# Optimization experiments

Measured on AMD Instinct MI355X. Metric: run time of the kernel, lower is better.

## Reference

```python
import jax, jax.numpy as jnp
import numpy as np
import math

B, NIN, DIM, QK, GS, L, BINS = 512, 128, 512, 128, 32, 2, 100
HID = int(DIM * 2.0)
G = NIN // GS
ROT = 32  # rotary dim = min(32, query_key_dim)
EPS = 1e-5


def setup_inputs() -> dict:
    key = jax.random.key(0)
    ks = jax.random.split(key, 8)
    r = jax.random.normal
    return {
        "tokens": jax.random.randint(ks[0], (B, NIN), 0, BINS),
        "emb": r(ks[1], (NIN, BINS, DIM), jnp.float32) * 0.02,
        "pos_emb": r(ks[2], (NIN, DIM), jnp.float32) * 0.01,
        "norm_g": jnp.ones((L,), jnp.float32),
        "Wh": r(ks[3], (L, DIM, 2 * HID), jnp.float32) / math.sqrt(DIM),
        "bh": jnp.zeros((L, 2 * HID), jnp.float32),
        "Wqk": r(ks[4], (L, DIM, QK), jnp.float32) / math.sqrt(DIM),
        "bqk": jnp.zeros((L, QK), jnp.float32),
        "gamma": r(ks[5], (L, 4, QK), jnp.float32) * 0.02,
        "beta": jnp.zeros((L, 4, QK), jnp.float32),
        "rp": r(ks[6], (L, 32), jnp.float32) * 0.02,
        "Wout": r(ks[7], (L, HID, DIM), jnp.float32) / math.sqrt(HID),
        "bout": jnp.zeros((L, DIM), jnp.float32),
        "ln_g": jnp.ones((DIM,), jnp.float32),
        "ln_b": jnp.zeros((DIM,), jnp.float32),
    }


def _t5_buckets(n, num_buckets=32, max_distance=128):
    # causal T5 relative position buckets, computed statically
    pos = np.arange(n)
    rel = pos[None, :] - pos[:, None]
    neg = np.maximum(-rel, 0)
    max_exact = num_buckets // 2
    vl = max_exact + (np.log(np.maximum(neg, 1) / max_exact) / np.log(max_distance / max_exact) * (num_buckets - max_exact)).astype(np.int64)
    vl = np.minimum(vl, num_buckets - 1)
    return jnp.asarray(np.where(neg < max_exact, neg, vl))


def _rotary_cos_sin(n):
    inv = 1.0 / (10000.0 ** (np.arange(0, ROT, 2) / ROT))
    f = np.einsum('i,j->ij', np.arange(n), inv)  # [n, ROT/2]
    f = np.repeat(f, 2, axis=-1)                 # interleaved-pair freqs [n, ROT]
    return jnp.asarray(np.cos(f), jnp.float32), jnp.asarray(np.sin(f), jnp.float32)


def _apply_rotary(x, cos, sin):
    xr, xp = x[..., :ROT], x[..., ROT:]
    x2 = xr.reshape(*xr.shape[:-1], ROT // 2, 2)
    rh = jnp.stack((-x2[..., 1], x2[..., 0]), axis=-1).reshape(xr.shape)
    return jnp.concatenate([xr * cos + rh * sin, xp], axis=-1)


def reference(tokens, emb, pos_emb, norm_g, Wh, bh, Wqk, bqk, gamma, beta, rp, Wout, bout, ln_g, ln_b):
    # per-column embedding lookup + positional embedding
    x = emb[jnp.arange(NIN)[None, :], tokens] + pos_emb  # [B, NIN, DIM]
    buckets = _t5_buckets(GS)
    cos, sin = _rotary_cos_sin(NIN)
    t5_scale = QK ** 0.5
    causal_mask = jnp.triu(jnp.ones((GS, GS), bool), 1)

    def grp(t):
        return t.reshape(B, G, GS, t.shape[-1])

    def layer(h, p):
        ng, Wh_l, bh_l, Wqk_l, bqk_l, gm, bt, rp_l, Wo_l, bo_l = p
        # ScaleNorm
        nrm = jnp.linalg.norm(h, axis=-1, keepdims=True) * DIM ** -0.5
        nx = h / jnp.maximum(nrm, EPS) * ng
        # shift_tokens: shift first half of features by one position
        xs, xp = nx[..., :DIM // 2], nx[..., DIM // 2:]
        xs = jnp.pad(xs, ((0, 0), (1, 0), (0, 0)))[:, :-1]
        nx = jnp.concatenate([xs, xp], axis=-1)
        hid = jax.nn.silu(nx @ Wh_l + bh_l)
        v, gate = hid[..., :HID], hid[..., HID:]
        qk = jax.nn.silu(nx @ Wqk_l + bqk_l)
        qs = qk[..., None, :] * gm + bt  # [B, NIN, 4, QK]
        quad_q = _apply_rotary(qs[..., 0, :], cos, sin)
        lin_q = _apply_rotary(qs[..., 1, :], cos, sin)
        quad_k = _apply_rotary(qs[..., 2, :], cos, sin)
        lin_k = _apply_rotary(qs[..., 3, :], cos, sin)
        qq, lq, kk, lk, vg = map(grp, (quad_q, lin_q, quad_k, lin_k, v))
        # grouped quadratic attention with ReLU^2 attn fn and T5 rel-pos bias
        sim = jnp.einsum('bgid,bgjd->bgij', qq, kk) / GS + rp_l[buckets] * t5_scale
        attn = jnp.square(jax.nn.relu(sim))
        attn = jnp.where(causal_mask, 0.0, attn)
        quad_out = jnp.einsum('bgij,bgje->bgie', attn, vg)
        # causal linear attention across groups (shifted cumsum of kv stats)
        lin_kv = jnp.einsum('bgnd,bgne->bgde', lk, vg) / GS
        lin_kv = jnp.cumsum(lin_kv, axis=1)
        lin_kv = jnp.pad(lin_kv, ((0, 0), (1, 0), (0, 0), (0, 0)))[:, :-1]
        lin_out = jnp.einsum('bgde,bgnd->bgne', lin_kv, lq)
        out = gate * (quad_out + lin_out).reshape(B, NIN, HID)
        return out @ Wo_l + bo_l + h, None

    x, _ = jax.lax.scan(layer, x, (norm_g, Wh, bh, Wqk, bqk, gamma, beta, rp, Wout, bout))
    mu = x.mean(-1, keepdims=True)
    var = x.var(-1, keepdims=True)
    return (x - mu) / jnp.sqrt(var + EPS) * ln_g + ln_b
```

## Files before the change

### kernel.cpp

```cpp
#include <hip/hip_runtime.h>
#include <hip/hip_bf16.h>
#include <math.h>
#include <stdint.h>

#define BB   512
#define NIN  128
#define DIMD 512
#define QKD  128
#define GSZ  32
#define GRP  4
#define HID  1024
#define HID2 2048
#define NFUSE 2176
#define ROT  32
#define NLAYER 2
#define EPSF 1e-5f
#define BINS 100

typedef __bf16 bf16x8 __attribute__((ext_vector_type(8)));
typedef float  f32x4  __attribute__((ext_vector_type(4)));
typedef float  f32x16 __attribute__((ext_vector_type(16)));

__device__ __forceinline__ unsigned short f2bf(float f) {
    union { float f; uint32_t u; } v; v.f = f;
    return (unsigned short)((v.u + 0x7FFFu + ((v.u >> 16) & 1u)) >> 16);
}
__device__ __forceinline__ float bf2f(unsigned short h) {
    union { uint32_t u; float f; } v; v.u = ((uint32_t)h) << 16;
    return v.f;
}

__global__ void k_embed(const int* __restrict__ tokens, const float* __restrict__ emb,
                        const float* __restrict__ pos, float* __restrict__ h) {
    int bn = blockIdx.x;
    int n  = bn % NIN;
    int tok = tokens[bn];
    const float4* e4 = (const float4*)(emb + ((size_t)n * BINS + tok) * DIMD);
    const float4* p4 = (const float4*)(pos + (size_t)n * DIMD);
    float4* h4 = (float4*)(h + (size_t)bn * DIMD);
    int t = threadIdx.x;
    float4 a = e4[t], b = p4[t];
    h4[t] = make_float4(a.x + b.x, a.y + b.y, a.z + b.z, a.w + b.w);
}

__global__ void k_nxf(const float* __restrict__ h, unsigned short* __restrict__ nx,
                      const float* __restrict__ ngp) {
    int bn = blockIdx.x; int n = bn % NIN;
    int t = threadIdx.x;
    float4 v = ((const float4*)(h + (size_t)bn * DIMD))[t];
    float sq = v.x * v.x + v.y * v.y + v.z * v.z + v.w * v.w;
    __shared__ float red[2];
    #pragma unroll
    for (int o = 32; o; o >>= 1) sq += __shfl_down(sq, o);
    int lane = t & 63, w = t >> 6;
    if (lane == 0) red[w] = sq;
    __syncthreads();
    float s = red[0] + red[1];
    float nrm = sqrtf(s) * (1.0f / sqrtf((float)DIMD));
    float sc = ngp[0] / fmaxf(nrm, EPSF);
    ushort4 o = make_ushort4(f2bf(v.x * sc), f2bf(v.y * sc), f2bf(v.z * sc), f2bf(v.w * sc));
    if (t < 64) {
        if (n == 0)
            ((ushort4*)(nx + (size_t)bn * DIMD))[t] = make_ushort4(0, 0, 0, 0);
        if (n != NIN - 1)
            ((ushort4*)(nx + (size_t)(bn + 1) * DIMD))[t] = o;
    } else {
        ((ushort4*)(nx + (size_t)bn * DIMD))[t] = o;
    }
}

__global__ void k_wcast(const float* __restrict__ W, unsigned short* __restrict__ Wt,
                        int K, int N) {
    int idx = blockIdx.x * 256 + threadIdx.x;
    int total = N * (K / 8);
    if (idx >= total) return;
    int kb = idx / N, n = idx % N;
    #pragma unroll
    for (int j = 0; j < 8; ++j)
        Wt[(size_t)n * K + kb * 8 + j] = f2bf(W[(size_t)(kb * 8 + j) * N + n]);
}

#define GLOAD_LDS(gp, lp) __builtin_amdgcn_global_load_lds( \
    (const __attribute__((address_space(1))) uint32_t*)(gp), \
    (__attribute__((address_space(3))) uint32_t*)(lp), 16, 0, 0)

__global__ __launch_bounds__(256) void k_gemm_f(
        const unsigned short* __restrict__ A,
        const unsigned short* __restrict__ Bt,
        const float* __restrict__ bias0,
        const float* __restrict__ bias1,
        float* __restrict__ Cf,
        unsigned short* __restrict__ vTp,
        unsigned short* __restrict__ gatep,
        int M, int N, int K) {
    __shared__ unsigned short As[3][128 * 32];
    __shared__ unsigned short Bs[3][128 * 32];
    const int tid = threadIdx.x;

    int flat = blockIdx.y * gridDim.x + blockIdx.x;
    int nwg  = gridDim.x * gridDim.y;
    int q = nwg >> 3, r = nwg & 7;
    int xcd = flat & 7, idx = flat >> 3;
    int swz = (xcd < r ? xcd * (q + 1) : r * (q + 1) + (xcd - r) * q) + idx;
    const int bxi = swz % gridDim.x, byi = swz / gridDim.x;
    const int bm = byi * 128, bn = bxi * 128;

    const int lane = tid & 63, wave = tid >> 6;
    const int wm = (wave >> 1) * 64, wn = (wave & 1) * 64;
    const int l15 = lane & 15, l4 = lane >> 4;

    f32x4 acc[4][4];
    #pragma unroll
    for (int i = 0; i < 4; ++i)
        #pragma unroll
        for (int j = 0; j < 4; ++j) acc[i][j] = (f32x4){0.f, 0.f, 0.f, 0.f};

    const int rowA = tid >> 2;
    const int colB = (tid & 3) * 16;
    const char* gA = (const char*)(A  + (size_t)(bm + rowA) * K) + colB;
    const char* gB = (const char*)(Bt + (size_t)(bn + rowA) * K) + colB;
    const size_t stride64 = (size_t)64 * K * 2;

    #define STAGEF(bi, k0) do { \
        const char* sA_ = gA + (size_t)(k0) * 2; \
        const char* sB_ = gB + (size_t)(k0) * 2; \
        GLOAD_LDS(sA_,            &As[bi][tid * 8]); \
        GLOAD_LDS(sA_ + stride64, &As[bi][tid * 8 + 2048]); \
        GLOAD_LDS(sB_,            &Bs[bi][tid * 8]); \
        GLOAD_LDS(sB_ + stride64, &Bs[bi][tid * 8 + 2048]); \
    } while (0)

    const int NIT = K / 32;
    STAGEF(0, 0);
    STAGEF(1, 32);

    int cur = 0;
    for (int t = 0; t < NIT; ++t) {
        asm volatile("s_waitcnt lgkmcnt(0)" ::: "memory");
        if (t + 1 < NIT) asm volatile("s_waitcnt vmcnt(4)" ::: "memory");
        else             asm volatile("s_waitcnt vmcnt(0)" ::: "memory");
        __builtin_amdgcn_s_barrier();

        if (t + 2 < NIT) {
            int tgt = cur + 2; if (tgt >= 3) tgt -= 3;
            STAGEF(tgt, (t + 2) * 32);
        }

        bf16x8 af[4], bfr[4];
        #pragma unroll
        for (int f = 0; f < 4; ++f) {
            af[f]  = *(const bf16x8*)&As[cur][(wm + f * 16 + l15) * 32 + l4 * 8];
            bfr[f] = *(const bf16x8*)&Bs[cur][(wn + f * 16 + l15) * 32 + l4 * 8];
        }
        __builtin_amdgcn_s_setprio(1);
        #pragma unroll
        for (int i = 0; i < 4; ++i)
            #pragma unroll
            for (int j = 0; j < 4; ++j)
                acc[i][j] = __builtin_amdgcn_mfma_f32_16x16x32_bf16(af[i], bfr[j], acc[i][j], 0, 0, 0);
        __builtin_amdgcn_s_setprio(0);

        cur = (cur == 2) ? 0 : cur + 1;
    }
    #undef STAGEF

    #pragma unroll
    for (int i = 0; i < 4; ++i) {
        const int n0 = wm + i * 16 + l4 * 4;
        #pragma unroll
        for (int j = 0; j < 4; ++j) {
            const int col = bn + wn + j * 16 + l15;
            float bsv = (col < 2 * HID) ? bias0[col] : bias1[col - 2 * HID];
            float vv[4];
            #pragma unroll
            for (int rr = 0; rr < 4; ++rr) {
                float v = acc[i][j][rr] + bsv;
                vv[rr] = v / (1.0f + __expf(-v));
            }
            if (col < HID) {
                ushort4 o = make_ushort4(f2bf(vv[0]), f2bf(vv[1]), f2bf(vv[2]), f2bf(vv[3]));
                *(ushort4*)&vTp[((size_t)byi * HID + col) * NIN + n0] = o;
            } else if (col < 2 * HID) {
                #pragma unroll
                for (int rr = 0; rr < 4; ++rr)
                    gatep[(size_t)(bm + n0 + rr) * HID + (col - HID)] = f2bf(vv[rr]);
            } else {
                #pragma unroll
                for (int rr = 0; rr < 4; ++rr)
                    Cf[(size_t)(bm + n0 + rr) * QKD + (col - 2 * HID)] = vv[rr];
            }
        }
    }
}

__global__ __launch_bounds__(256, 2) void k_gemm_o(
        const unsigned short* __restrict__ A,
        const unsigned short* __restrict__ Bt,
        const float* __restrict__ bias0,
        const float* __restrict__ resid,
        float* __restrict__ Cf,
        int M, int N, int K) {
    __shared__ unsigned short As[2][256 * 32];
    __shared__ unsigned short Bs[2][128 * 32];
    const int tid = threadIdx.x;

    int flat = blockIdx.y * gridDim.x + blockIdx.x;
    int nwg  = gridDim.x * gridDim.y;
    int q = nwg >> 3, r = nwg & 7;
    int xcd = flat & 7, idx = flat >> 3;
    int swz = (xcd < r ? xcd * (q + 1) : r * (q + 1) + (xcd - r) * q) + idx;
    const int bxi = swz % gridDim.x, byi = swz / gridDim.x;
    const int bm = byi * 256, bn = bxi * 128;

    const int lane = tid & 63, wave = tid >> 6;
    const int l15 = lane & 15, l4 = lane >> 4;

    f32x4 acc[4][8];
    #pragma unroll
    for (int i = 0; i < 4; ++i)
        #pragma unroll
        for (int j = 0; j < 8; ++j) acc[i][j] = (f32x4){0.f, 0.f, 0.f, 0.f};

    const int rowA = tid >> 2;
    const int colO = (tid & 3) * 16;
    const int colS = colO ^ ((rowA & 3) << 4);
    const char* gA = (const char*)(A  + (size_t)(bm + rowA) * K) + colS;
    const char* gB = (const char*)(Bt + (size_t)(bn + rowA) * K) + colS;
    const size_t stride64 = (size_t)64 * K * 2;

    #define STAGEO(bi, k0) do { \
        const char* sA_ = gA + (size_t)(k0) * 2; \
        const char* sB_ = gB + (size_t)(k0) * 2; \
        GLOAD_LDS(sA_,                 &As[bi][tid * 8]); \
        GLOAD_LDS(sA_ +     stride64,  &As[bi][tid * 8 + 2048]); \
        GLOAD_LDS(sA_ + 2 * stride64,  &As[bi][tid * 8 + 4096]); \
        GLOAD_LDS(sA_ + 3 * stride64,  &As[bi][tid * 8 + 6144]); \
        GLOAD_LDS(sB_,                 &Bs[bi][tid * 8]); \
        GLOAD_LDS(sB_ +     stride64,  &Bs[bi][tid * 8 + 2048]); \
    } while (0)

    const int NIT = K / 32;
    STAGEO(0, 0);
    STAGEO(1, 32);

    for (int t = 0; t < NIT; ++t) {
        const int cur = t & 1;
        if (t + 1 < NIT) asm volatile("s_waitcnt vmcnt(6)" ::: "memory");
        else             asm volatile("s_waitcnt vmcnt(0)" ::: "memory");
        __builtin_amdgcn_s_barrier();
        __builtin_amdgcn_sched_barrier(0);

        bf16x8 af[4], bfr[8];
        #pragma unroll
        for (int f = 0; f < 4; ++f) {
            int rA = wave * 64 + f * 16 + l15;
            af[f] = *(const bf16x8*)&As[cur][rA * 32 + ((l4 ^ (rA & 3)) << 3)];
        }
        #pragma unroll
        for (int c = 0; c < 8; ++c) {
            int rB = c * 16 + l15;
            bfr[c] = *(const bf16x8*)&Bs[cur][rB * 32 + ((l4 ^ (rB & 3)) << 3)];
        }
        asm volatile("s_waitcnt lgkmcnt(0)" ::: "memory");
        __builtin_amdgcn_sched_barrier(0);
        __builtin_amdgcn_s_barrier();
        __builtin_amdgcn_sched_barrier(0);
        if (t + 2 < NIT) STAGEO(cur, (t + 2) * 32);

        __builtin_amdgcn_s_setprio(1);
        #pragma unroll
        for (int f = 0; f < 4; ++f)
            #pragma unroll
            for (int c = 0; c < 8; ++c)
                acc[f][c] = __builtin_amdgcn_mfma_f32_16x16x32_bf16(af[f], bfr[c], acc[f][c], 0, 0, 0);
        __builtin_amdgcn_s_setprio(0);
    }
    #undef STAGEO

    #pragma unroll
    for (int f = 0; f < 4; ++f) {
        const int n0 = wave * 64 + f * 16 + l4 * 4;
        #pragma unroll
        for (int c = 0; c < 8; ++c) {
            const int col = bn + c * 16 + l15;
            float bsv = bias0[col];
            #pragma unroll
            for (int rr = 0; rr < 4; ++rr) {
                size_t row = bm + n0 + rr;
                Cf[row * N + col] = acc[f][c][rr] + bsv + resid[row * N + col];
            }
        }
    }
}

__global__ void k_cossin(float* __restrict__ cosb, float* __restrict__ sinb) {
    int idx = blockIdx.x * 256 + threadIdx.x;
    if (idx >= NIN * 16) return;
    int n = idx / 16, i = idx % 16;
    double inv = pow(10000.0, -(double)(2 * i) / (double)ROT);
    double f = (double)n * inv;
    cosb[idx] = (float)cos(f);
    sinb[idx] = (float)sin(f);
}

__global__ void k_rot(const float* __restrict__ qk, const float* __restrict__ gm,
                      const float* __restrict__ bt, const float* __restrict__ cosb,
                      const float* __restrict__ sinb, unsigned short* __restrict__ q4) {
    int bn = blockIdx.x; int n = bn % NIN;
    int d = threadIdx.x;
    float x = qk[(size_t)bn * QKD + d];
    float xp0 = 0.f;
    int dp = d ^ 1;
    if (d < ROT) xp0 = qk[(size_t)bn * QKD + dp];
    #pragma unroll
    for (int c = 0; c < 4; ++c) {
        float val = x * gm[c * QKD + d] + bt[c * QKD + d];
        float outv;
        if (d < ROT) {
            int i = d >> 1;
            float cs = cosb[n * 16 + i], sn = sinb[n * 16 + i];
            float xp = xp0 * gm[c * QKD + dp] + bt[c * QKD + dp];
            outv = ((d & 1) == 0) ? (val * cs - xp * sn) : (val * cs + xp * sn);
        } else outv = val;
        q4[((size_t)bn * 4 + c) * QKD + d] = f2bf(outv);
    }
}

__global__ __launch_bounds__(256) void k_attn2(
        const unsigned short* __restrict__ q4,
        const unsigned short* __restrict__ gatep,
        const unsigned short* __restrict__ vT,
        const float* __restrict__ rp,
        unsigned short* __restrict__ attn_out) {
    int et = blockIdx.x, b = blockIdx.y;
    int tid = threadIdx.x, wave = tid >> 6, lane = tid & 63;
    int l31 = lane & 31, lhi = lane >> 5;

    __shared__ unsigned short S[32][136];
    __shared__ float rps_d[32];
    if (tid < 32) {
        int d = tid, bucket;
        if (d < 16) bucket = d;
        else {
            bucket = 16 + (int)(logf((float)d * (1.0f / 16.0f)) * (16.0f / logf(8.0f)));
            if (bucket > 31) bucket = 31;
        }
        rps_d[tid] = rp[bucket] * sqrtf((float)QKD);
    }
    __syncthreads();

    size_t bbase = (size_t)b * NIN;
    int e0 = et * 256 + wave * 64;
    const unsigned short* vbase = vT + (size_t)b * HID * NIN;

    for (int g = 0; g < GRP; ++g) {
        if (wave <= g) {
            int gp = wave;
            bool quad = (gp == g);
            const unsigned short* Qb = q4 + ((bbase + g  * 32 + l31) * 4 + (quad ? 0 : 1)) * QKD;
            const unsigned short* Kb = q4 + ((bbase + gp * 32 + l31) * 4 + (quad ? 2 : 3)) * QKD;
            f32x16 sa = {};
            #pragma unroll
            for (int kk = 0; kk < 8; ++kk) {
                bf16x8 aq = *(const bf16x8*)(Qb + kk * 16 + lhi * 8);
                bf16x8 bk = *(const bf16x8*)(Kb + kk * 16 + lhi * 8);
                sa = __builtin_amdgcn_mfma_f32_32x32x16_bf16(aq, bk, sa, 0, 0, 0);
            }
            int j = l31;
            #pragma unroll
            for (int r = 0; r < 16; ++r) {
                int i = (r & 3) + 8 * (r >> 2) + 4 * lhi;
                float s = sa[r] * (1.0f / GSZ);
                if (quad) {
                    if (j > i) s = 0.f;
                    else {
                        s += rps_d[i - j];
                        s = fmaxf(s, 0.f);
                        s = s * s;
                    }
                }
                S[i][gp * 32 + j] = f2bf(s);
            }
        }
        __syncthreads();

        f32x16 o0 = {}, o1 = {};
        int KT = 2 * (g + 1);
        for (int kk = 0; kk < KT; ++kk) {
            int k0 = kk * 16 + lhi * 8;
            bf16x8 af = *(const bf16x8*)&S[l31][k0];
            bf16x8 b0 = *(const bf16x8*)(vbase + (size_t)(e0 + l31) * NIN + k0);
            bf16x8 b1 = *(const bf16x8*)(vbase + (size_t)(e0 + 32 + l31) * NIN + k0);
            o0 = __builtin_amdgcn_mfma_f32_32x32x16_bf16(af, b0, o0, 0, 0, 0);
            o1 = __builtin_amdgcn_mfma_f32_32x32x16_bf16(af, b1, o1, 0, 0, 0);
        }
        __syncthreads();

        int ea = e0 + l31, eb = e0 + 32 + l31;
        #pragma unroll
        for (int r = 0; r < 16; ++r) {
            int i = (r & 3) + 8 * (r >> 2) + 4 * lhi;
            size_t row = bbase + g * 32 + i;
            float ga = bf2f(gatep[row * HID + ea]);
            float gb = bf2f(gatep[row * HID + eb]);
            attn_out[row * HID + ea] = f2bf(ga * o0[r]);
            attn_out[row * HID + eb] = f2bf(gb * o1[r]);
        }
    }
}

__global__ void k_ln(const float* __restrict__ h, const float* __restrict__ lng,
                     const float* __restrict__ lnb, float* __restrict__ out) {
    int bn = blockIdx.x;
    int t = threadIdx.x;
    const float4* r4 = (const float4*)(h + (size_t)bn * DIMD);
    float4 v = r4[t];
    float s  = v.x + v.y + v.z + v.w;
    float sq = v.x * v.x + v.y * v.y + v.z * v.z + v.w * v.w;
    __shared__ float red[4];
    #pragma unroll
    for (int o = 32; o; o >>= 1) { s += __shfl_down(s, o); sq += __shfl_down(sq, o); }
    int lane = t & 63, w = t >> 6;
    if (lane == 0) { red[w] = s; red[2 + w] = sq; }
    __syncthreads();
    float mu  = (red[0] + red[1]) * (1.0f / DIMD);
    float var = (red[2] + red[3]) * (1.0f / DIMD) - mu * mu;
    float rstd = 1.0f / sqrtf(var + EPSF);
    float4 gg = ((const float4*)lng)[t];
    float4 bb = ((const float4*)lnb)[t];
    float4 o;
    o.x = (v.x - mu) * rstd * gg.x + bb.x;
    o.y = (v.y - mu) * rstd * gg.y + bb.y;
    o.z = (v.z - mu) * rstd * gg.z + bb.z;
    o.w = (v.w - mu) * rstd * gg.w + bb.w;
    ((float4*)(out + (size_t)bn * DIMD))[t] = o;
}

extern "C" void kernel_launch(void* const* d_in, const int* in_sizes, int n_in,
                              void* d_out, int out_size, void* d_ws, size_t ws_size,
                              hipStream_t stream) {
    const int*   tokens = (const int*)d_in[0];
    const float* emb    = (const float*)d_in[1];
    const float* pos    = (const float*)d_in[2];
    const float* norm_g = (const float*)d_in[3];
    const float* Wh     = (const float*)d_in[4];
    const float* bh     = (const float*)d_in[5];
    const float* Wqk    = (const float*)d_in[6];
    const float* bqk    = (const float*)d_in[7];
    const float* gamma  = (const float*)d_in[8];
    const float* beta   = (const float*)d_in[9];
    const float* rp     = (const float*)d_in[10];
    const float* Wout   = (const float*)d_in[11];
    const float* bout   = (const float*)d_in[12];
    const float* lng    = (const float*)d_in[13];
    const float* lnb    = (const float*)d_in[14];

    float* h  = (float*)d_out;
    float* ws = (float*)d_ws;

    size_t off = 0;
    float* cosb  = ws + off; off += NIN * 16;
    float* sinb  = ws + off; off += NIN * 16;
    unsigned short* whqkT = (unsigned short*)(ws + off); off += (size_t)NLAYER * NFUSE * DIMD / 2;
    unsigned short* woutT = (unsigned short*)(ws + off); off += (size_t)NLAYER * DIMD * HID / 2;
    off = (off + 63) & ~(size_t)63;
    const size_t fixedFloats = off;

    const size_t wsFloats = ws_size / sizeof(float);
    const size_t perBatch = (size_t)NIN * (DIMD / 2 + HID / 2 + HID / 2 + QKD + DIMD / 2 + HID / 2);
    int CB = BB;
    while (CB > 2 && fixedFloats + (size_t)CB * perBatch + 64 > wsFloats) CB >>= 1;

    unsigned short* nx    = (unsigned short*)(ws + off); off += (size_t)CB * NIN * DIMD / 2;
    unsigned short* vT    = (unsigned short*)(ws + off); off += (size_t)CB * HID * NIN / 2;
    unsigned short* gateB = (unsigned short*)(ws + off); off += (size_t)CB * NIN * HID / 2;
    float*          qk    = ws + off;                    off += (size_t)CB * NIN * QKD;
    unsigned short* q4    = (unsigned short*)(ws + off); off += (size_t)CB * NIN * DIMD / 2;
    unsigned short* attnB = (unsigned short*)(ws + off); off += (size_t)CB * NIN * HID / 2;

    const int BN_ = BB * NIN;

    k_cossin<<<8, 256, 0, stream>>>(cosb, sinb);
    k_embed<<<BN_, 128, 0, stream>>>(tokens, emb, pos, h);

    for (int l = 0; l < NLAYER; ++l) {
        unsigned short* whqkT_l = whqkT + (size_t)l * NFUSE * DIMD;
        k_wcast<<<(HID2 * DIMD / 8 + 255) / 256, 256, 0, stream>>>(
            Wh + (size_t)l * DIMD * HID2,  whqkT_l, DIMD, HID2);
        k_wcast<<<(QKD * DIMD / 8 + 255) / 256, 256, 0, stream>>>(
            Wqk + (size_t)l * DIMD * QKD,  whqkT_l + (size_t)HID2 * DIMD, DIMD, QKD);
        k_wcast<<<(DIMD * HID / 8 + 255) / 256, 256, 0, stream>>>(
            Wout + (size_t)l * HID * DIMD, woutT + (size_t)l * DIMD * HID, HID, DIMD);
    }

    for (int l = 0; l < NLAYER; ++l) {
        const float* bh_l  = bh   + (size_t)l * HID2;
        const float* bqk_l = bqk  + (size_t)l * QKD;
        const float* gm_l  = gamma+ (size_t)l * 4 * QKD;
        const float* bt_l  = beta + (size_t)l * 4 * QKD;
        const float* rp_l  = rp   + (size_t)l * 32;
        const float* bo_l  = bout + (size_t)l * DIMD;
        const unsigned short* whqkT_l = whqkT + (size_t)l * NFUSE * DIMD;
        const unsigned short* woutT_l = woutT + (size_t)l * DIMD * HID;

        for (int c0 = 0; c0 < BB; c0 += CB) {
            const int rowsC = CB * NIN;
            float* h_c = h + (size_t)c0 * NIN * DIMD;

            k_nxf<<<rowsC, 128, 0, stream>>>(h_c, nx, norm_g + l);

            dim3 g1(NFUSE / 128, rowsC / 128);
            k_gemm_f<<<g1, 256, 0, stream>>>(nx, whqkT_l, bh_l, bqk_l,
                                             qk, vT, gateB, rowsC, NFUSE, DIMD);

            k_rot<<<rowsC, 128, 0, stream>>>(qk, gm_l, bt_l, cosb, sinb, q4);

            dim3 ga(HID / 256, CB);
            k_attn2<<<ga, 256, 0, stream>>>(q4, gateB, vT, rp_l, attnB);

            dim3 g3(DIMD / 128, rowsC / 256);
            k_gemm_o<<<g3, 256, 0, stream>>>(attnB, woutT_l, bo_l, h_c, h_c,
                                             rowsC, DIMD, HID);
        }
    }

    k_ln<<<BN_, 128, 0, stream>>>(h, lng, lnb, (float*)d_out);
}
```

Baseline: 1.365 ms.

## Fuse rotary/scale-offset into fused GEMM epilogue and use double-buffered K loop

Removes the separate k_rot kernel and the fp32 qk workspace. The blocks of the fused GEMM that own the QK columns now apply SiLU, the per-head gamma/beta scale-offset and rotary embedding in the epilogue, using a lane shuffle to fetch the pair element, and write bf16 q4 directly. The K-loop drops from triple to double buffering, with a second barrier before reissuing loads into the buffer just consumed, and the setprio hints are removed. This saves a kernel launch and the qk round trip through memory. In exchange, those epilogue blocks become heavier and issue many scattered 2-byte stores, and the two-stage pipeline may hide memory latency less well.

```diff
diff --git a/kernel.cpp b/kernel.cpp
--- a/kernel.cpp
+++ b/kernel.cpp
@@ -89,12 +89,16 @@
         const unsigned short* __restrict__ Bt,
         const float* __restrict__ bias0,
         const float* __restrict__ bias1,
-        float* __restrict__ Cf,
+        const float* __restrict__ gm,
+        const float* __restrict__ bt,
+        const float* __restrict__ cosb,
+        const float* __restrict__ sinb,
+        unsigned short* __restrict__ q4,
         unsigned short* __restrict__ vTp,
         unsigned short* __restrict__ gatep,
         int M, int N, int K) {
-    __shared__ unsigned short As[3][128 * 32];
-    __shared__ unsigned short Bs[3][128 * 32];
+    __shared__ unsigned short As[2][128 * 32];
+    __shared__ unsigned short Bs[2][128 * 32];
     const int tid = threadIdx.x;
 
     int flat = blockIdx.y * gridDim.x + blockIdx.x;
@@ -134,17 +138,12 @@
     STAGEF(0, 0);
     STAGEF(1, 32);
 
-    int cur = 0;
     for (int t = 0; t < NIT; ++t) {
-        asm volatile("s_waitcnt lgkmcnt(0)" ::: "memory");
+        const int cur = t & 1;
         if (t + 1 < NIT) asm volatile("s_waitcnt vmcnt(4)" ::: "memory");
         else             asm volatile("s_waitcnt vmcnt(0)" ::: "memory");
         __builtin_amdgcn_s_barrier();
-
-        if (t + 2 < NIT) {
-            int tgt = cur + 2; if (tgt >= 3) tgt -= 3;
-            STAGEF(tgt, (t + 2) * 32);
-        }
+        __builtin_amdgcn_sched_barrier(0);
 
         bf16x8 af[4], bfr[4];
         #pragma unroll
@@ -152,42 +151,77 @@
             af[f]  = *(const bf16x8*)&As[cur][(wm + f * 16 + l15) * 32 + l4 * 8];
             bfr[f] = *(const bf16x8*)&Bs[cur][(wn + f * 16 + l15) * 32 + l4 * 8];
         }
-        __builtin_amdgcn_s_setprio(1);
+        asm volatile("s_waitcnt lgkmcnt(0)" ::: "memory");
+        __builtin_amdgcn_sched_barrier(0);
+        __builtin_amdgcn_s_barrier();
+        __builtin_amdgcn_sched_barrier(0);
+        if (t + 2 < NIT) STAGEF(cur, (t + 2) * 32);
+
         #pragma unroll
         for (int i = 0; i < 4; ++i)
             #pragma unroll
             for (int j = 0; j < 4; ++j)
                 acc[i][j] = __builtin_amdgcn_mfma_f32_16x16x32_bf16(af[i], bfr[j], acc[i][j], 0, 0, 0);
-        __builtin_amdgcn_s_setprio(0);
-
-        cur = (cur == 2) ? 0 : cur + 1;
     }
     #undef STAGEF
 
-    #pragma unroll
-    for (int i = 0; i < 4; ++i) {
-        const int n0 = wm + i * 16 + l4 * 4;
-        #pragma unroll
-        for (int j = 0; j < 4; ++j) {
-            const int col = bn + wn + j * 16 + l15;
-            float bsv = (col < 2 * HID) ? bias0[col] : bias1[col - 2 * HID];
-            float vv[4];
-            #pragma unroll
-            for (int rr = 0; rr < 4; ++rr) {
-                float v = acc[i][j][rr] + bsv;
-                vv[rr] = v / (1.0f + __expf(-v));
+    if (bn == 2 * HID) {
+        #pragma unroll
+        for (int i = 0; i < 4; ++i) {
+            const int n0 = wm + i * 16 + l4 * 4;
+            #pragma unroll
+            for (int j = 0; j < 4; ++j) {
+                const int d = wn + j * 16 + l15;
+                float bsv = bias1[d];
+                float vv[4];
+                #pragma unroll
+                for (int rr = 0; rr < 4; ++rr) {
+                    float v = acc[i][j][rr] + bsv;
+                    vv[rr] = v / (1.0f + __expf(-v));
+                }
+                const bool rot = (wn == 0) && (j < 2);
+                #pragma unroll
+                for (int c = 0; c < 4; ++c) {
+                    float gmv = gm[c * QKD + d], btv = bt[c * QKD + d];
+                    #pragma unroll
+                    for (int rr = 0; rr < 4; ++rr) {
+                        float val = vv[rr] * gmv + btv;
+                        float outv = val;
+                        if (rot) {
+                            float prt = __shfl_xor(val, 1);
+                            int n = n0 + rr;
+                            float cs = cosb[n * 16 + (d >> 1)];
+                            float sn = sinb[n * 16 + (d >> 1)];
+                            outv = ((d & 1) == 0) ? (val * cs - prt * sn)
+                                                  : (val * cs + prt * sn);
+                        }
+                        q4[((size_t)(bm + n0 + rr) * 4 + c) * QKD + d] = f2bf(outv);
+                    }
+                }
             }
-            if (col < HID) {
-                ushort4 o = make_ushort4(f2bf(vv[0]), f2bf(vv[1]), f2bf(vv[2]), f2bf(vv[3]));
-                *(ushort4*)&vTp[((size_t)byi * HID + col) * NIN + n0] = o;
-            } else if (col < 2 * HID) {
+        }
+    } else {
+        #pragma unroll
+        for (int i = 0; i < 4; ++i) {
+            const int n0 = wm + i * 16 + l4 * 4;
+            #pragma unroll
+            for (int j = 0; j < 4; ++j) {
+                const int col = bn + wn + j * 16 + l15;
+                float bsv = bias0[col];
+                float vv[4];
                 #pragma unroll
-                for (int rr = 0; rr < 4; ++rr)
-                    gatep[(size_t)(bm + n0 + rr) * HID + (col - HID)] = f2bf(vv[rr]);
-            } else {
-                #pragma unroll
-                for (int rr = 0; rr < 4; ++rr)
-                    Cf[(size_t)(bm + n0 + rr) * QKD + (col - 2 * HID)] = vv[rr];
+                for (int rr = 0; rr < 4; ++rr) {
+                    float v = acc[i][j][rr] + bsv;
+                    vv[rr] = v / (1.0f + __expf(-v));
+                }
+                if (col < HID) {
+                    ushort4 o = make_ushort4(f2bf(vv[0]), f2bf(vv[1]), f2bf(vv[2]), f2bf(vv[3]));
+                    *(ushort4*)&vTp[((size_t)byi * HID + col) * NIN + n0] = o;
+                } else {
+                    #pragma unroll
+                    for (int rr = 0; rr < 4; ++rr)
+                        gatep[(size_t)(bm + n0 + rr) * HID + (col - HID)] = f2bf(vv[rr]);
+                }
             }
         }
     }
@@ -301,29 +335,6 @@
     double f = (double)n * inv;
     cosb[idx] = (float)cos(f);
     sinb[idx] = (float)sin(f);
-}
-
-__global__ void k_rot(const float* __restrict__ qk, const float* __restrict__ gm,
-                      const float* __restrict__ bt, const float* __restrict__ cosb,
-                      const float* __restrict__ sinb, unsigned short* __restrict__ q4) {
-    int bn = blockIdx.x; int n = bn % NIN;
-    int d = threadIdx.x;
-    float x = qk[(size_t)bn * QKD + d];
-    float xp0 = 0.f;
-    int dp = d ^ 1;
-    if (d < ROT) xp0 = qk[(size_t)bn * QKD + dp];
-    #pragma unroll
-    for (int c = 0; c < 4; ++c) {
-        float val = x * gm[c * QKD + d] + bt[c * QKD + d];
-        float outv;
-        if (d < ROT) {
-            int i = d >> 1;
-            float cs = cosb[n * 16 + i], sn = sinb[n * 16 + i];
-            float xp = xp0 * gm[c * QKD + dp] + bt[c * QKD + dp];
-            outv = ((d & 1) == 0) ? (val * cs - xp * sn) : (val * cs + xp * sn);
-        } else outv = val;
-        q4[((size_t)bn * 4 + c) * QKD + d] = f2bf(outv);
-    }
 }
 
 __global__ __launch_bounds__(256) void k_attn2(
@@ -467,14 +478,13 @@
     const size_t fixedFloats = off;
 
     const size_t wsFloats = ws_size / sizeof(float);
-    const size_t perBatch = (size_t)NIN * (DIMD / 2 + HID / 2 + HID / 2 + QKD + DIMD / 2 + HID / 2);
+    const size_t perBatch = (size_t)NIN * (DIMD / 2 + HID / 2 + HID / 2 + DIMD / 2 + HID / 2);
     int CB = BB;
     while (CB > 2 && fixedFloats + (size_t)CB * perBatch + 64 > wsFloats) CB >>= 1;
 
     unsigned short* nx    = (unsigned short*)(ws + off); off += (size_t)CB * NIN * DIMD / 2;
     unsigned short* vT    = (unsigned short*)(ws + off); off += (size_t)CB * HID * NIN / 2;
     unsigned short* gateB = (unsigned short*)(ws + off); off += (size_t)CB * NIN * HID / 2;
-    float*          qk    = ws + off;                    off += (size_t)CB * NIN * QKD;
     unsigned short* q4    = (unsigned short*)(ws + off); off += (size_t)CB * NIN * DIMD / 2;
     unsigned short* attnB = (unsigned short*)(ws + off); off += (size_t)CB * NIN * HID / 2;
 
@@ -511,9 +521,8 @@
 
             dim3 g1(NFUSE / 128, rowsC / 128);
             k_gemm_f<<<g1, 256, 0, stream>>>(nx, whqkT_l, bh_l, bqk_l,
-                                             qk, vT, gateB, rowsC, NFUSE, DIMD);
-
-            k_rot<<<rowsC, 128, 0, stream>>>(qk, gm_l, bt_l, cosb, sinb, q4);
+                                             gm_l, bt_l, cosb, sinb,
+                                             q4, vT, gateB, rowsC, NFUSE, DIMD);
 
             dim3 ga(HID / 256, CB);
             k_attn2<<<ga, 256, 0, stream>>>(q4, gateB, vT, rp_l, attnB);
```

Result: slower. 1.432 ms (+4.9%).
